# Optimization experiments

Hardware: AMD Instinct MI355X
Metric: run time of the kernel (lower is better)

The kernel has to match this reference:

```python
import jax, jax.numpy as jnp
import numpy as np

D_MODEL = 1024
NUM_HEADS = 16
D_K = D_MODEL // NUM_HEADS
B, L = 2, 2048
DTYPE = jnp.bfloat16


def setup_inputs() -> dict:
    key = jax.random.key(0)
    k1, k2, k3 = jax.random.split(key, 3)
    x = jax.random.normal(k1, (B, L, D_MODEL), dtype=DTYPE)
    # causal mask (B, 1, L, L): True = keep
    mask = jnp.broadcast_to(jnp.tril(jnp.ones((L, L), dtype=bool)), (B, 1, L, L))
    W_qkv = (jax.random.normal(k2, (D_MODEL, 3 * D_MODEL), dtype=jnp.float32) * (D_MODEL ** -0.5)).astype(DTYPE)
    W_out = (jax.random.normal(k3, (D_MODEL, D_MODEL), dtype=jnp.float32) * (D_MODEL ** -0.5)).astype(DTYPE)
    return {"x": x, "mask": mask, "W_qkv": W_qkv, "W_out": W_out}


def reference(x, mask, W_qkv, W_out):
    b, l, d = x.shape
    scale = jax.lax.rsqrt(jnp.array(D_K, dtype=DTYPE))
    qkv = jnp.einsum('bld,de->ble', x, W_qkv)            # (B, L, 3*D)
    qkv = qkv.reshape(b, l, 3, NUM_HEADS, D_K)
    qkv = jnp.transpose(qkv, (2, 0, 3, 1, 4))            # (3, B, H, L, d_k)
    q, k, v = qkv[0], qkv[1], qkv[2]
    logits = jnp.einsum('bhqd,bhkd->bhqk', q, k) * scale  # (B, H, L, L)
    neg_inf = jnp.array(-1e9, dtype=logits.dtype)
    logits = jnp.where(mask, logits, neg_inf)
    attn = jax.nn.softmax(logits.astype(jnp.float32), axis=-1).astype(DTYPE)
    ctx = jnp.einsum('bhqk,bhkd->bhqd', attn, v)          # (B, H, L, d_k)
    ctx = jnp.transpose(ctx, (0, 2, 1, 3)).reshape(b, l, d)
    return jnp.einsum('bld,de->ble', ctx, W_out)
```

## Files before the change

kernel.cpp:

```cpp
#include <hip/hip_runtime.h>
#include <hip/hip_bf16.h>

typedef __bf16 bf16x8 __attribute__((ext_vector_type(8)));
typedef float f32x4 __attribute__((ext_vector_type(4)));
typedef unsigned short u16;

#define MFMA16(a, b, c) __builtin_amdgcn_mfma_f32_16x16x32_bf16((a), (b), (c), 0, 0, 0)

typedef __attribute__((address_space(1))) void glb_void;
typedef __attribute__((address_space(3))) void lds_void;

__device__ __forceinline__ void gload16(const void* g, void* l) {
    __builtin_amdgcn_global_load_lds((glb_void*)g, (lds_void*)l, 16, 0, 0);
}

__device__ __forceinline__ float bf2f(u16 h) {
    union { unsigned int u; float f; } v;
    v.u = ((unsigned int)h) << 16;
    return v.f;
}
__device__ __forceinline__ u16 f2bf(float f) {
    union { float f; unsigned int u; } v;
    v.f = f;
    unsigned int r = v.u + 0x7fffu + ((v.u >> 16) & 1u);
    return (u16)(r >> 16);
}
__device__ __forceinline__ float bfround(float f) { return bf2f(f2bf(f)); }
__device__ __forceinline__ u16 f2bf_n(float f) {
    union { __bf16 h; u16 u; } t; t.h = (__bf16)f; return t.u;
}
__device__ __forceinline__ float bfrd(float f) { return (float)(__bf16)f; }


__global__ __launch_bounds__(256) void MultiHeadSelfAttention_11759620456627_probe(
    const u16* p0, const u16* p1, const u16* p2, const u16* p3, const u16* p4, const u16* p5,
    int s0, int s1, int s2, int s3, int s4, int s5,
    int n_in, unsigned long long wsbytes, u16* ws) {
    const int tid = threadIdx.x;
    if (tid >= 64) return;
    unsigned long long* ctl = (unsigned long long*)ws;
    const u16* ptrs[6] = {p0, p1, p2, p3, p4, p5};
    long long szs[6] = {s0, s1, s2, s3, s4, s5};
    int cls[6];
    const u16* xp = 0;
    int xf = 0, ncx = 0, ncw = 0;
    const u16* wp[2] = {0, 0};
    long long wsz[2] = {0, 0};
    int wf[2] = {0, 0};
    const size_t lane = (size_t)tid;
    for (int i = 0; i < 6; ++i) {
        cls[i] = 3;
        if (i >= n_in || ptrs[i] == 0 || szs[i] < 1048576) continue;
        u16 a = ptrs[i][lane * 8191 + 1];
        float fa = fabsf(bf2f(a));
        float vb = ((const float*)(const void*)ptrs[i])[lane * 4093 + 1];
        float fb = fabsf(vb);
        const int nmask  = __popcll(__ballot(a == 0 || a == 1 || a == 256 || a == 257 || a == 0x3F80));
        const int plausA = __popcll(__ballot(fa > 0.0005f && fa < 64.0f));
        const int plausB = __popcll(__ballot(fb > 0.0005f && fb < 64.0f));
        const int bigA   = __popcll(__ballot(fa >= 0.125f && fa < 64.0f));
        const int bigB   = __popcll(__ballot(fb >= 0.125f && fb < 64.0f));
        if (nmask >= 60) { cls[i] = 0; continue; }
        const int isf = (plausB > plausA) ? 1 : 0;
        const int big = isf ? bigB : bigA;
        if (big >= 16) { cls[i] = 2; xp = ptrs[i]; xf = isf; ++ncx; }
        else {
            cls[i] = 1;
            if (ncw < 2) { wp[ncw] = ptrs[i]; wsz[ncw] = szs[i]; wf[ncw] = isf; }
            ++ncw;
        }
    }
    if (tid != 0) return;
    const u16 *wq = 0, *wo = 0;
    int qf = 0, of = 0, ok = 0;
    if (ncx == 1 && ncw == 2) {
        if (wsz[0] == 3 * wsz[1])      { wq = wp[0]; qf = wf[0]; wo = wp[1]; of = wf[1]; ok = 1; }
        else if (wsz[1] == 3 * wsz[0]) { wq = wp[1]; qf = wf[1]; wo = wp[0]; of = wf[0]; ok = 1; }
    }
    const int wsok = (wsbytes >= 128ull + 23068672ull) ? 1 : 0;
    if (!wsok) ok = 0;
    float code = 0.0f;
    if (!ok) {
        if (!wsok) code = 6144.0f;
        else if (ncx == 1 && ncw == 2) code = 5120.0f;
        else code = 2048.0f + 8.0f * (float)(cls[0] + 4 * cls[1] + 16 * cls[2] + 64 * cls[3]);
    }
    ctl[0] = (unsigned long long)xp;
    ctl[1] = (unsigned long long)wq;
    ctl[2] = (unsigned long long)wo;
    ctl[3] = (unsigned long long)ok;
    ctl[4] = (unsigned long long)(xf | (qf << 1) | (of << 2));
    union { float f; unsigned int u; } cv; cv.f = code;
    ctl[5] = (unsigned long long)cv.u;
}

__global__ __launch_bounds__(256) void MultiHeadSelfAttention_11759620456627_selftest(u16* ws) {
    unsigned long long* ctl = (unsigned long long*)ws;
    if (ctl[3] == 0ull) return;
    __shared__ __align__(16) u16 At[512];
    __shared__ __align__(16) u16 Bt2[512];
    __shared__ int flagv;
    const int tid = threadIdx.x;
    if (tid == 0) flagv = 0;
    if (tid < 64)
        for (int i = tid; i < 512; i += 64) {
            int m = i >> 5, k = i & 31;
            At[i]  = f2bf((float)((m * 3 + k) % 7 - 3) * 0.25f);
            Bt2[i] = f2bf((float)((m + 2 * k) % 5 - 2) * 0.25f);
        }
    __syncthreads();
    if (tid < 64) {
        const int l16 = tid & 15, quad = tid >> 4;
        bf16x8 a = *(bf16x8*)&At[l16 * 32 + quad * 8];
        bf16x8 b = *(bf16x8*)&Bt2[l16 * 32 + quad * 8];
        f32x4 c = {0.f, 0.f, 0.f, 0.f};
        c = MFMA16(a, b, c);
        for (int r = 0; r < 4; ++r) {
            const int row = quad * 4 + r, col = l16;
            float ref = 0.f;
            for (int k = 0; k < 32; ++k) ref += bf2f(At[row * 32 + k]) * bf2f(Bt2[col * 32 + k]);
            if (fabsf(c[r] - ref) > 1e-3f) { *(volatile int*)&flagv = 1; }
        }
    }
    __syncthreads();
    if (tid == 0 && flagv) {
        ctl[3] = 0ull;
        union { float f; unsigned int u; } cv; cv.f = 10240.0f;
        ctl[5] = (unsigned long long)cv.u;
    }
}

__global__ __launch_bounds__(256) void MultiHeadSelfAttention_11759620456627_convx(u16* ws) {
    unsigned long long* ctl = (unsigned long long*)ws;
    if (ctl[3] == 0ull) return;
    u16* base = ws + 64;
    const u16* x = (const u16*)ctl[0];
    const int xf = (int)(ctl[4] & 1ull);
    const size_t i0 = ((size_t)(blockIdx.x * 256 + threadIdx.x)) * 8;
    if (!xf) {
        *(int4*)&base[i0] = *(const int4*)&x[i0];
    } else {
        const float* xp = (const float*)(const void*)x;
        float4 a = *(const float4*)&xp[i0];
        float4 bb = *(const float4*)&xp[i0 + 4];
        union { u16 h[8]; int4 v; } t;
        t.h[0] = f2bf(a.x);  t.h[1] = f2bf(a.y);  t.h[2] = f2bf(a.z);  t.h[3] = f2bf(a.w);
        t.h[4] = f2bf(bb.x); t.h[5] = f2bf(bb.y); t.h[6] = f2bf(bb.z); t.h[7] = f2bf(bb.w);
        *(int4*)&base[i0] = t.v;
    }
}

__global__ __launch_bounds__(256) void MultiHeadSelfAttention_11759620456627_transw(u16* ws, int which) {
    unsigned long long* ctl = (unsigned long long*)ws;
    if (ctl[3] == 0ull) return;
    __shared__ __align__(16) u16 t[64][72];
    const int tid = threadIdx.x;
    const u16* src = (const u16*)(which ? ctl[2] : ctl[1]);
    const int flag = which ? (int)((ctl[4] >> 2) & 1ull) : (int)((ctl[4] >> 1) & 1ull);
    const int C = which ? 1024 : 3072;
    const int R = 1024;
    u16* dst = ws + 64 + 4194304;
    const int r0 = blockIdx.y * 64, c0 = blockIdx.x * 64;
    for (int idx = tid; idx < 512; idx += 256) {
        const int r = idx >> 3, c8 = (idx & 7) * 8;
        const size_t o = (size_t)(r0 + r) * C + c0 + c8;
        if (!flag) {
            *(int4*)&t[r][c8] = *(const int4*)&src[o];
        } else {
            const float* sf = (const float*)(const void*)src;
            float4 a = *(const float4*)&sf[o];
            float4 bb = *(const float4*)&sf[o + 4];
            u16* d = &t[r][c8];
            d[0] = f2bf(a.x);  d[1] = f2bf(a.y);  d[2] = f2bf(a.z);  d[3] = f2bf(a.w);
            d[4] = f2bf(bb.x); d[5] = f2bf(bb.y); d[6] = f2bf(bb.z); d[7] = f2bf(bb.w);
        }
    }
    __syncthreads();
    for (int idx = tid; idx < 512; idx += 256) {
        const int r = idx >> 3, c8 = (idx & 7) * 8;
        union { u16 h[8]; int4 v; } tmp;
#pragma unroll
        for (int j = 0; j < 8; ++j) tmp.h[j] = t[c8 + j][r];
        *(int4*)&dst[(size_t)(c0 + r) * R + r0 + c8] = tmp.v;
    }
}

__global__ __launch_bounds__(256) void MultiHeadSelfAttention_11759620456627_qkv(u16* out, u16* ws) {
    unsigned long long* ctl = (unsigned long long*)ws;
    if (ctl[3] == 0ull) return;
    __shared__ __align__(16) u16 As[4096];
    __shared__ __align__(16) u16 Bs[4096];
    const u16* A  = ws + 64;
    const u16* Bt = ws + 64 + 4194304;
    u16* vt = ws + 64 + 7340032;
    u16* qb = out;
    u16* kb = out + 4194304;
    const int K = 1024;
    const int tid = threadIdx.x;
    const int wave = tid >> 6, lane = tid & 63;
    const int quad = lane >> 4, l16 = lane & 15;
    const int m0 = blockIdx.y * 128, n0 = blockIdx.x * 128;
    const int wr = (wave >> 1) * 64, wc = (wave & 1) * 64;
    f32x4 acc[4][4] = {};
    const int rl = wave * 16 + (lane >> 2), cl = (lane & 3) * 8;
    const u16* a0 = A  + (size_t)(m0 + rl) * K + cl;
    const u16* a1 = A  + (size_t)(m0 + 64 + rl) * K + cl;
    const u16* b0 = Bt + (size_t)(n0 + rl) * K + cl;
    const u16* b1 = Bt + (size_t)(n0 + 64 + rl) * K + cl;
    u16* lA0 = As + wave * 512;
    u16* lA1 = As + 2048 + wave * 512;
    u16* lB0 = Bs + wave * 512;
    u16* lB1 = Bs + 2048 + wave * 512;
    for (int kb2 = 0; kb2 < K; kb2 += 32) {
        gload16(a0 + kb2, lA0);
        gload16(a1 + kb2, lA1);
        gload16(b0 + kb2, lB0);
        gload16(b1 + kb2, lB1);
        __syncthreads();
        bf16x8 af[4], bfr[4];
#pragma unroll
        for (int i = 0; i < 4; ++i) af[i] = *(const bf16x8*)&As[(wr + i * 16 + l16) * 32 + quad * 8];
#pragma unroll
        for (int j = 0; j < 4; ++j) bfr[j] = *(const bf16x8*)&Bs[(wc + j * 16 + l16) * 32 + quad * 8];
#pragma unroll
        for (int i = 0; i < 4; ++i)
#pragma unroll
            for (int j = 0; j < 4; ++j) acc[i][j] = MFMA16(af[i], bfr[j], acc[i][j]);
        __syncthreads();
    }
#pragma unroll
    for (int i = 0; i < 4; ++i)
#pragma unroll
        for (int j = 0; j < 4; ++j) {
            const int col = n0 + wc + j * 16 + l16;
            const int s = col >> 10, rem = col & 1023;
            const int h = rem >> 6, d = rem & 63;
#pragma unroll
            for (int r = 0; r < 4; ++r) {
                const int row = m0 + wr + i * 16 + quad * 4 + r;
                const int b = row >> 11, l = row & 2047;
                const int bh = b * 16 + h;
                const u16 val = f2bf(acc[i][j][r]);
                if (s == 0)      qb[((size_t)bh * 2048 + l) * 64 + d] = val;
                else if (s == 1) kb[((size_t)bh * 2048 + l) * 64 + d] = val;
                else             vt[((size_t)bh * 64 + d) * 2048 + l] = val;
            }
        }
}

__global__ __launch_bounds__(256) void MultiHeadSelfAttention_11759620456627_attn(u16* out, u16* ws) {
    unsigned long long* ctl = (unsigned long long*)ws;
    if (ctl[3] == 0ull) return;
    constexpr int L = 2048, DK = 64, PAD = 72;
    constexpr float C1 = 0.18033688011112042f;
    constexpr float C2 = -11.541560327111708f;
    __shared__ __align__(16) u16 Ks[64 * PAD];
    __shared__ __align__(16) u16 Vs[64 * PAD];
    __shared__ __align__(16) u16 Pl[4 * 16 * PAD];
    u16* base = ws + 64;
    u16* vt   = ws + 64 + 7340032;
    u16* qb   = out;
    u16* kb   = out + 4194304;
    const int tid = threadIdx.x;
    const int wave = tid >> 6, lane = tid & 63;
    const int quad = lane >> 4, l16 = lane & 15;
    const int bid = (int)blockIdx.x;
    const int bh = (bid & 7) * 4 + (bid >> 7);
    const int pairx = (bid >> 3) & 15;
    const u16* Qp = qb + (size_t)bh * L * DK;
    const u16* Kp = kb + (size_t)bh * L * DK;
    const u16* Vp = vt + (size_t)bh * DK * L;
    u16* Pw = &Pl[wave * 16 * PAD];
    const int b = bh >> 4, h = bh & 15;
    const int srow = tid >> 3, scol = (tid & 7) * 8;

    for (int half = 0; half < 2; ++half) {
        const int qt = half == 0 ? pairx : 31 - pairx;
        const int q0 = qt * 64 + wave * 16;
        const bf16x8 qf0 = *(const bf16x8*)&Qp[(size_t)(q0 + l16) * DK + quad * 8];
        const bf16x8 qf1 = *(const bf16x8*)&Qp[(size_t)(q0 + l16) * DK + quad * 8 + 32];
        f32x4 oacc[4] = {};
        float lpart[4] = {0.f, 0.f, 0.f, 0.f};

        for (int kc = 0; kc <= qt; ++kc) {
            const int k0 = kc * 64;
            __syncthreads();
#pragma unroll
            for (int it = 0; it < 2; ++it) {
                const int r = srow + it * 32;
                *(int4*)&Ks[r * PAD + scol] = *(const int4*)&Kp[(size_t)(k0 + r) * DK + scol];
                *(int4*)&Vs[r * PAD + scol] = *(const int4*)&Vp[(size_t)r * L + k0 + scol];
            }
            __syncthreads();
            const bool maskchunk = (kc == qt);
            f32x4 sacc[4];
#pragma unroll
            for (int kt = 0; kt < 4; ++kt) {
                const bf16x8 kf0 = *(const bf16x8*)&Ks[(kt * 16 + l16) * PAD + quad * 8];
                const bf16x8 kf1 = *(const bf16x8*)&Ks[(kt * 16 + l16) * PAD + quad * 8 + 32];
                f32x4 z = {0.f, 0.f, 0.f, 0.f};
                z = MFMA16(qf0, kf0, z);
                sacc[kt] = MFMA16(qf1, kf1, z);
            }
#pragma unroll
            for (int kt = 0; kt < 4; ++kt)
#pragma unroll
                for (int r = 0; r < 4; ++r) {
                    float s = bfrd(sacc[kt][r]);
                    if (maskchunk) {
                        const int key = k0 + kt * 16 + l16;
                        const int qrow = q0 + quad * 4 + r;
                        if (key > qrow) s = -3.0e38f;
                    }
                    const float pv = exp2f(__builtin_fmaf(s, C1, C2));
                    lpart[r] += pv;
                    Pw[(quad * 4 + r) * PAD + kt * 16 + l16] = f2bf_n(pv);
                }
            const bf16x8 pa0 = *(const bf16x8*)&Pw[l16 * PAD + quad * 8];
            const bf16x8 pa1 = *(const bf16x8*)&Pw[l16 * PAD + quad * 8 + 32];
#pragma unroll
            for (int nt = 0; nt < 4; ++nt) {
                const bf16x8 vf0 = *(const bf16x8*)&Vs[(nt * 16 + l16) * PAD + quad * 8];
                const bf16x8 vf1 = *(const bf16x8*)&Vs[(nt * 16 + l16) * PAD + quad * 8 + 32];
                oacc[nt] = MFMA16(pa0, vf0, oacc[nt]);
                oacc[nt] = MFMA16(pa1, vf1, oacc[nt]);
            }
        }
        float linv[4];
#pragma unroll
        for (int r = 0; r < 4; ++r) {
            float ls = lpart[r];
#pragma unroll
            for (int off = 1; off < 16; off <<= 1) ls += __shfl_xor(ls, off);
            linv[r] = 1.0f / ls;
        }
#pragma unroll
        for (int nt = 0; nt < 4; ++nt)
#pragma unroll
            for (int r = 0; r < 4; ++r) {
                const int q = q0 + quad * 4 + r;
                base[((size_t)b * 2048 + q) * 1024 + h * 64 + nt * 16 + l16] =
                    f2bf_n(oacc[nt][r] * linv[r]);
            }
    }
}

__global__ __launch_bounds__(256) void MultiHeadSelfAttention_11759620456627_outp(u16* out, u16* ws) {
    unsigned long long* ctl = (unsigned long long*)ws;
    const int tid = threadIdx.x;
    if (ctl[3] == 0ull) {
        union { unsigned int u; float f; } cv; cv.u = (unsigned int)ctl[5];
        float* outf = (float*)(void*)out;
        const int bid = blockIdx.y * gridDim.x + blockIdx.x;
        for (int k = 0; k < 64; ++k)
            outf[(size_t)(bid * 256 + tid) + (size_t)k * 65536] = cv.f;
        return;
    }
    __shared__ __align__(16) u16 As[4096];
    __shared__ __align__(16) u16 Bs[4096];
    const u16* A  = ws + 64;
    const u16* Bt = ws + 64 + 4194304;
    const int K = 1024;
    const int wave = tid >> 6, lane = tid & 63;
    const int quad = lane >> 4, l16 = lane & 15;
    const int m0 = blockIdx.y * 128, n0 = blockIdx.x * 128;
    const int wr = (wave >> 1) * 64, wc = (wave & 1) * 64;
    f32x4 acc[4][4] = {};
    const int rl = wave * 16 + (lane >> 2), cl = (lane & 3) * 8;
    const u16* a0 = A  + (size_t)(m0 + rl) * K + cl;
    const u16* a1 = A  + (size_t)(m0 + 64 + rl) * K + cl;
    const u16* b0 = Bt + (size_t)(n0 + rl) * K + cl;
    const u16* b1 = Bt + (size_t)(n0 + 64 + rl) * K + cl;
    u16* lA0 = As + wave * 512;
    u16* lA1 = As + 2048 + wave * 512;
    u16* lB0 = Bs + wave * 512;
    u16* lB1 = Bs + 2048 + wave * 512;
    for (int kb2 = 0; kb2 < K; kb2 += 32) {
        gload16(a0 + kb2, lA0);
        gload16(a1 + kb2, lA1);
        gload16(b0 + kb2, lB0);
        gload16(b1 + kb2, lB1);
        __syncthreads();
        bf16x8 af[4], bfr[4];
#pragma unroll
        for (int i = 0; i < 4; ++i) af[i] = *(const bf16x8*)&As[(wr + i * 16 + l16) * 32 + quad * 8];
#pragma unroll
        for (int j = 0; j < 4; ++j) bfr[j] = *(const bf16x8*)&Bs[(wc + j * 16 + l16) * 32 + quad * 8];
#pragma unroll
        for (int i = 0; i < 4; ++i)
#pragma unroll
            for (int j = 0; j < 4; ++j) acc[i][j] = MFMA16(af[i], bfr[j], acc[i][j]);
        __syncthreads();
    }
    float* outf = (float*)(void*)out;
#pragma unroll
    for (int i = 0; i < 4; ++i)
#pragma unroll
        for (int j = 0; j < 4; ++j) {
            const int col = n0 + wc + j * 16 + l16;
#pragma unroll
            for (int r = 0; r < 4; ++r) {
                const int row = m0 + wr + i * 16 + quad * 4 + r;
                outf[(size_t)row * 1024 + col] = bfround(acc[i][j][r]);
            }
        }
}

extern "C" void kernel_launch(void* const* d_in, const int* in_sizes, int n_in,
                              void* d_out, int out_size, void* d_ws, size_t ws_size,
                              hipStream_t stream) {
    (void)out_size;
    const u16* p[6] = {0, 0, 0, 0, 0, 0};
    int s[6] = {-1, -1, -1, -1, -1, -1};
    for (int i = 0; i < n_in && i < 6; ++i) { p[i] = (const u16*)d_in[i]; s[i] = in_sizes[i]; }
    u16* out = (u16*)d_out;
    u16* ws  = (u16*)d_ws;
    const unsigned long long wsbytes = (unsigned long long)ws_size;

    MultiHeadSelfAttention_11759620456627_probe<<<dim3(1, 1), 256, 0, stream>>>(
        p[0], p[1], p[2], p[3], p[4], p[5], s[0], s[1], s[2], s[3], s[4], s[5],
        n_in, wsbytes, ws);
    MultiHeadSelfAttention_11759620456627_selftest<<<dim3(1, 1), 256, 0, stream>>>(ws);
    MultiHeadSelfAttention_11759620456627_convx<<<dim3(2048, 1), 256, 0, stream>>>(ws);
    MultiHeadSelfAttention_11759620456627_transw<<<dim3(48, 16), 256, 0, stream>>>(ws, 0);
    MultiHeadSelfAttention_11759620456627_qkv<<<dim3(24, 32), 256, 0, stream>>>(out, ws);
    MultiHeadSelfAttention_11759620456627_transw<<<dim3(16, 16), 256, 0, stream>>>(ws, 1);
    MultiHeadSelfAttention_11759620456627_attn<<<dim3(512, 1), 256, 0, stream>>>(out, ws);
    MultiHeadSelfAttention_11759620456627_outp<<<dim3(8, 32), 256, 0, stream>>>(out, ws);
}
```

Measured before the change: 243.9 us.

## Deepen GEMM K-tile to 64 and split attention pairs into separate blocks

The QKV and output-projection GEMMs now stage 64-wide K slices per iteration instead of 32, doubling LDS tiles and halving the number of barriers and load rounds. The attention kernel no longer processes a balanced pair of query tiles per block. It launches 1024 blocks, one query tile each, with a rotated tile-to-block mapping meant to keep the causal workload spread evenly. This raises parallelism and occupancy, but loses the built-in load balancing of pairing and doubles the LDS used by the GEMMs.

Measured after the change: 263.0 us. 7.8% more time.

```diff
diff --git a/kernel.cpp b/kernel.cpp
--- a/kernel.cpp
+++ b/kernel.cpp
@@ -188,8 +188,8 @@
 __global__ __launch_bounds__(256) void MultiHeadSelfAttention_11759620456627_qkv(u16* out, u16* ws) {
     unsigned long long* ctl = (unsigned long long*)ws;
     if (ctl[3] == 0ull) return;
-    __shared__ __align__(16) u16 As[4096];
-    __shared__ __align__(16) u16 Bs[4096];
+    __shared__ __align__(16) u16 As[8192];
+    __shared__ __align__(16) u16 Bs[8192];
     const u16* A  = ws + 64;
     const u16* Bt = ws + 64 + 4194304;
     u16* vt = ws + 64 + 7340032;
@@ -202,30 +202,27 @@
     const int m0 = blockIdx.y * 128, n0 = blockIdx.x * 128;
     const int wr = (wave >> 1) * 64, wc = (wave & 1) * 64;
     f32x4 acc[4][4] = {};
-    const int rl = wave * 16 + (lane >> 2), cl = (lane & 3) * 8;
-    const u16* a0 = A  + (size_t)(m0 + rl) * K + cl;
-    const u16* a1 = A  + (size_t)(m0 + 64 + rl) * K + cl;
-    const u16* b0 = Bt + (size_t)(n0 + rl) * K + cl;
-    const u16* b1 = Bt + (size_t)(n0 + 64 + rl) * K + cl;
-    u16* lA0 = As + wave * 512;
-    u16* lA1 = As + 2048 + wave * 512;
-    u16* lB0 = Bs + wave * 512;
-    u16* lB1 = Bs + 2048 + wave * 512;
-    for (int kb2 = 0; kb2 < K; kb2 += 32) {
-        gload16(a0 + kb2, lA0);
-        gload16(a1 + kb2, lA1);
-        gload16(b0 + kb2, lB0);
-        gload16(b1 + kb2, lB1);
-        __syncthreads();
-        bf16x8 af[4], bfr[4];
-#pragma unroll
-        for (int i = 0; i < 4; ++i) af[i] = *(const bf16x8*)&As[(wr + i * 16 + l16) * 32 + quad * 8];
-#pragma unroll
-        for (int j = 0; j < 4; ++j) bfr[j] = *(const bf16x8*)&Bs[(wc + j * 16 + l16) * 32 + quad * 8];
-#pragma unroll
-        for (int i = 0; i < 4; ++i)
-#pragma unroll
-            for (int j = 0; j < 4; ++j) acc[i][j] = MFMA16(af[i], bfr[j], acc[i][j]);
+    const int rl = lane >> 3, cl = (lane & 7) * 8;
+    for (int kb2 = 0; kb2 < K; kb2 += 64) {
+#pragma unroll
+        for (int q = 0; q < 4; ++q) {
+            const int row = wave * 32 + q * 8 + rl;
+            gload16(A  + (size_t)(m0 + row) * K + kb2 + cl, As + (wave * 4 + q) * 512);
+            gload16(Bt + (size_t)(n0 + row) * K + kb2 + cl, Bs + (wave * 4 + q) * 512);
+        }
+        __syncthreads();
+#pragma unroll
+        for (int kk = 0; kk < 64; kk += 32) {
+            bf16x8 af[4], bfr[4];
+#pragma unroll
+            for (int i = 0; i < 4; ++i) af[i] = *(const bf16x8*)&As[(wr + i * 16 + l16) * 64 + kk + quad * 8];
+#pragma unroll
+            for (int j = 0; j < 4; ++j) bfr[j] = *(const bf16x8*)&Bs[(wc + j * 16 + l16) * 64 + kk + quad * 8];
+#pragma unroll
+            for (int i = 0; i < 4; ++i)
+#pragma unroll
+                for (int j = 0; j < 4; ++j) acc[i][j] = MFMA16(af[i], bfr[j], acc[i][j]);
+        }
         __syncthreads();
     }
 #pragma unroll
@@ -265,8 +262,11 @@
     const int wave = tid >> 6, lane = tid & 63;
     const int quad = lane >> 4, l16 = lane & 15;
     const int bid = (int)blockIdx.x;
-    const int bh = (bid & 7) * 4 + (bid >> 7);
-    const int pairx = (bid >> 3) & 15;
+    const int x = bid & 7, j = bid >> 3;
+    const int t = j >> 5, c = j & 31;
+    const int bh = x * 4 + t;
+    const int c2 = (c + ((t >> 1) << 4)) & 31;
+    const int qt = (t & 1) ? c2 : 31 - c2;
     const u16* Qp = qb + (size_t)bh * L * DK;
     const u16* Kp = kb + (size_t)bh * L * DK;
     const u16* Vp = vt + (size_t)bh * DK * L;
@@ -274,75 +274,72 @@
     const int b = bh >> 4, h = bh & 15;
     const int srow = tid >> 3, scol = (tid & 7) * 8;
 
-    for (int half = 0; half < 2; ++half) {
-        const int qt = half == 0 ? pairx : 31 - pairx;
-        const int q0 = qt * 64 + wave * 16;
-        const bf16x8 qf0 = *(const bf16x8*)&Qp[(size_t)(q0 + l16) * DK + quad * 8];
-        const bf16x8 qf1 = *(const bf16x8*)&Qp[(size_t)(q0 + l16) * DK + quad * 8 + 32];
-        f32x4 oacc[4] = {};
-        float lpart[4] = {0.f, 0.f, 0.f, 0.f};
-
-        for (int kc = 0; kc <= qt; ++kc) {
-            const int k0 = kc * 64;
-            __syncthreads();
-#pragma unroll
-            for (int it = 0; it < 2; ++it) {
-                const int r = srow + it * 32;
-                *(int4*)&Ks[r * PAD + scol] = *(const int4*)&Kp[(size_t)(k0 + r) * DK + scol];
-                *(int4*)&Vs[r * PAD + scol] = *(const int4*)&Vp[(size_t)r * L + k0 + scol];
+    const int q0 = qt * 64 + wave * 16;
+    const bf16x8 qf0 = *(const bf16x8*)&Qp[(size_t)(q0 + l16) * DK + quad * 8];
+    const bf16x8 qf1 = *(const bf16x8*)&Qp[(size_t)(q0 + l16) * DK + quad * 8 + 32];
+    f32x4 oacc[4] = {};
+    float lpart[4] = {0.f, 0.f, 0.f, 0.f};
+
+    for (int kc = 0; kc <= qt; ++kc) {
+        const int k0 = kc * 64;
+        __syncthreads();
+#pragma unroll
+        for (int it = 0; it < 2; ++it) {
+            const int r = srow + it * 32;
+            *(int4*)&Ks[r * PAD + scol] = *(const int4*)&Kp[(size_t)(k0 + r) * DK + scol];
+            *(int4*)&Vs[r * PAD + scol] = *(const int4*)&Vp[(size_t)r * L + k0 + scol];
+        }
+        __syncthreads();
+        const bool maskchunk = (kc == qt);
+        f32x4 sacc[4];
+#pragma unroll
+        for (int kt = 0; kt < 4; ++kt) {
+            const bf16x8 kf0 = *(const bf16x8*)&Ks[(kt * 16 + l16) * PAD + quad * 8];
+            const bf16x8 kf1 = *(const bf16x8*)&Ks[(kt * 16 + l16) * PAD + quad * 8 + 32];
+            f32x4 z = {0.f, 0.f, 0.f, 0.f};
+            z = MFMA16(qf0, kf0, z);
+            sacc[kt] = MFMA16(qf1, kf1, z);
+        }
+#pragma unroll
+        for (int kt = 0; kt < 4; ++kt)
+#pragma unroll
+            for (int r = 0; r < 4; ++r) {
+                float s = bfrd(sacc[kt][r]);
+                if (maskchunk) {
+                    const int key = k0 + kt * 16 + l16;
+                    const int qrow = q0 + quad * 4 + r;
+                    if (key > qrow) s = -3.0e38f;
+                }
+                const float pv = exp2f(__builtin_fmaf(s, C1, C2));
+                lpart[r] += pv;
+                Pw[(quad * 4 + r) * PAD + kt * 16 + l16] = f2bf_n(pv);
             }
-            __syncthreads();
-            const bool maskchunk = (kc == qt);
-            f32x4 sacc[4];
-#pragma unroll
-            for (int kt = 0; kt < 4; ++kt) {
-                const bf16x8 kf0 = *(const bf16x8*)&Ks[(kt * 16 + l16) * PAD + quad * 8];
-                const bf16x8 kf1 = *(const bf16x8*)&Ks[(kt * 16 + l16) * PAD + quad * 8 + 32];
-                f32x4 z = {0.f, 0.f, 0.f, 0.f};
-                z = MFMA16(qf0, kf0, z);
-                sacc[kt] = MFMA16(qf1, kf1, z);
-            }
-#pragma unroll
-            for (int kt = 0; kt < 4; ++kt)
-#pragma unroll
-                for (int r = 0; r < 4; ++r) {
-                    float s = bfrd(sacc[kt][r]);
-                    if (maskchunk) {
-                        const int key = k0 + kt * 16 + l16;
-                        const int qrow = q0 + quad * 4 + r;
-                        if (key > qrow) s = -3.0e38f;
-                    }
-                    const float pv = exp2f(__builtin_fmaf(s, C1, C2));
-                    lpart[r] += pv;
-                    Pw[(quad * 4 + r) * PAD + kt * 16 + l16] = f2bf_n(pv);
-                }
-            const bf16x8 pa0 = *(const bf16x8*)&Pw[l16 * PAD + quad * 8];
-            const bf16x8 pa1 = *(const bf16x8*)&Pw[l16 * PAD + quad * 8 + 32];
-#pragma unroll
-            for (int nt = 0; nt < 4; ++nt) {
-                const bf16x8 vf0 = *(const bf16x8*)&Vs[(nt * 16 + l16) * PAD + quad * 8];
-                const bf16x8 vf1 = *(const bf16x8*)&Vs[(nt * 16 + l16) * PAD + quad * 8 + 32];
-                oacc[nt] = MFMA16(pa0, vf0, oacc[nt]);
-                oacc[nt] = MFMA16(pa1, vf1, oacc[nt]);
-            }
-        }
-        float linv[4];
+        const bf16x8 pa0 = *(const bf16x8*)&Pw[l16 * PAD + quad * 8];
+        const bf16x8 pa1 = *(const bf16x8*)&Pw[l16 * PAD + quad * 8 + 32];
+#pragma unroll
+        for (int nt = 0; nt < 4; ++nt) {
+            const bf16x8 vf0 = *(const bf16x8*)&Vs[(nt * 16 + l16) * PAD + quad * 8];
+            const bf16x8 vf1 = *(const bf16x8*)&Vs[(nt * 16 + l16) * PAD + quad * 8 + 32];
+            oacc[nt] = MFMA16(pa0, vf0, oacc[nt]);
+            oacc[nt] = MFMA16(pa1, vf1, oacc[nt]);
+        }
+    }
+    float linv[4];
+#pragma unroll
+    for (int r = 0; r < 4; ++r) {
+        float ls = lpart[r];
+#pragma unroll
+        for (int off = 1; off < 16; off <<= 1) ls += __shfl_xor(ls, off);
+        linv[r] = 1.0f / ls;
+    }
+#pragma unroll
+    for (int nt = 0; nt < 4; ++nt)
 #pragma unroll
         for (int r = 0; r < 4; ++r) {
-            float ls = lpart[r];
-#pragma unroll
-            for (int off = 1; off < 16; off <<= 1) ls += __shfl_xor(ls, off);
-            linv[r] = 1.0f / ls;
-        }
-#pragma unroll
-        for (int nt = 0; nt < 4; ++nt)
-#pragma unroll
-            for (int r = 0; r < 4; ++r) {
-                const int q = q0 + quad * 4 + r;
-                base[((size_t)b * 2048 + q) * 1024 + h * 64 + nt * 16 + l16] =
-                    f2bf_n(oacc[nt][r] * linv[r]);
-            }
-    }
+            const int q = q0 + quad * 4 + r;
+            base[((size_t)b * 2048 + q) * 1024 + h * 64 + nt * 16 + l16] =
+                f2bf_n(oacc[nt][r] * linv[r]);
+        }
 }
 
 __global__ __launch_bounds__(256) void MultiHeadSelfAttention_11759620456627_outp(u16* out, u16* ws) {
@@ -356,8 +353,8 @@
             outf[(size_t)(bid * 256 + tid) + (size_t)k * 65536] = cv.f;
         return;
     }
-    __shared__ __align__(16) u16 As[4096];
-    __shared__ __align__(16) u16 Bs[4096];
+    __shared__ __align__(16) u16 As[8192];
+    __shared__ __align__(16) u16 Bs[8192];
     const u16* A  = ws + 64;
     const u16* Bt = ws + 64 + 4194304;
     const int K = 1024;
@@ -366,30 +363,27 @@
     const int m0 = blockIdx.y * 128, n0 = blockIdx.x * 128;
     const int wr = (wave >> 1) * 64, wc = (wave & 1) * 64;
     f32x4 acc[4][4] = {};
-    const int rl = wave * 16 + (lane >> 2), cl = (lane & 3) * 8;
-    const u16* a0 = A  + (size_t)(m0 + rl) * K + cl;
-    const u16* a1 = A  + (size_t)(m0 + 64 + rl) * K + cl;
-    const u16* b0 = Bt + (size_t)(n0 + rl) * K + cl;
-    const u16* b1 = Bt + (size_t)(n0 + 64 + rl) * K + cl;
-    u16* lA0 = As + wave * 512;
-    u16* lA1 = As + 2048 + wave * 512;
-    u16* lB0 = Bs + wave * 512;
-    u16* lB1 = Bs + 2048 + wave * 512;
-    for (int kb2 = 0; kb2 < K; kb2 += 32) {
-        gload16(a0 + kb2, lA0);
-        gload16(a1 + kb2, lA1);
-        gload16(b0 + kb2, lB0);
-        gload16(b1 + kb2, lB1);
-        __syncthreads();
-        bf16x8 af[4], bfr[4];
-#pragma unroll
-        for (int i = 0; i < 4; ++i) af[i] = *(const bf16x8*)&As[(wr + i * 16 + l16) * 32 + quad * 8];
-#pragma unroll
-        for (int j = 0; j < 4; ++j) bfr[j] = *(const bf16x8*)&Bs[(wc + j * 16 + l16) * 32 + quad * 8];
-#pragma unroll
-        for (int i = 0; i < 4; ++i)
-#pragma unroll
-            for (int j = 0; j < 4; ++j) acc[i][j] = MFMA16(af[i], bfr[j], acc[i][j]);
+    const int rl = lane >> 3, cl = (lane & 7) * 8;
+    for (int kb2 = 0; kb2 < K; kb2 += 64) {
+#pragma unroll
+        for (int q = 0; q < 4; ++q) {
+            const int row = wave * 32 + q * 8 + rl;
+            gload16(A  + (size_t)(m0 + row) * K + kb2 + cl, As + (wave * 4 + q) * 512);
+            gload16(Bt + (size_t)(n0 + row) * K + kb2 + cl, Bs + (wave * 4 + q) * 512);
+        }
+        __syncthreads();
+#pragma unroll
+        for (int kk = 0; kk < 64; kk += 32) {
+            bf16x8 af[4], bfr[4];
+#pragma unroll
+            for (int i = 0; i < 4; ++i) af[i] = *(const bf16x8*)&As[(wr + i * 16 + l16) * 64 + kk + quad * 8];
+#pragma unroll
+            for (int j = 0; j < 4; ++j) bfr[j] = *(const bf16x8*)&Bs[(wc + j * 16 + l16) * 64 + kk + quad * 8];
+#pragma unroll
+            for (int i = 0; i < 4; ++i)
+#pragma unroll
+                for (int j = 0; j < 4; ++j) acc[i][j] = MFMA16(af[i], bfr[j], acc[i][j]);
+        }
         __syncthreads();
     }
     float* outf = (float*)(void*)out;
@@ -425,6 +419,6 @@
     MultiHeadSelfAttention_11759620456627_transw<<<dim3(48, 16), 256, 0, stream>>>(ws, 0);
     MultiHeadSelfAttention_11759620456627_qkv<<<dim3(24, 32), 256, 0, stream>>>(out, ws);
     MultiHeadSelfAttention_11759620456627_transw<<<dim3(16, 16), 256, 0, stream>>>(ws, 1);
-    MultiHeadSelfAttention_11759620456627_attn<<<dim3(512, 1), 256, 0, stream>>>(out, ws);
+    MultiHeadSelfAttention_11759620456627_attn<<<dim3(1024, 1), 256, 0, stream>>>(out, ws);
     MultiHeadSelfAttention_11759620456627_outp<<<dim3(8, 32), 256, 0, stream>>>(out, ws);
 }
```
